# Optimization experiments

Hardware: AMD Instinct MI355X
Metric: run time of the kernel (lower is better)

The kernel has to match this reference:

```python
import jax, jax.numpy as jnp
from jax import lax
import numpy as np

L = 21                      # total_labels (incl. background class 0)
VARIANCES = (0.1, 0.1, 0.2, 0.2)
NMS_THRESHOLD = 0.5
MAX_TOTAL_SIZE = 200        # also max_output_size_per_class
SCORE_THRESHOLD = 0.5


def setup_inputs() -> dict:
    key = jax.random.key(0)
    k1, k2, k3, k4 = jax.random.split(key, 4)
    B, N = 1, 2048
    # valid normalized rois: y1<y2, x1<x2, inside [0,1]
    yx = jax.random.uniform(k1, (B, N, 2)) * 0.8
    hw = jax.random.uniform(k2, (B, N, 2)) * 0.19 + 0.01
    roi_bboxes = jnp.concatenate([yx, yx + hw], axis=-1)
    pred_deltas = jax.random.normal(k3, (B, N, L * 4)) * 0.2
    pred_label_probs = jax.random.uniform(k4, (B, N, L))
    return {"roi_bboxes": roi_bboxes, "pred_deltas": pred_deltas,
            "pred_label_probs": pred_label_probs}


def _decode(rois, deltas):
    # rois/deltas: (..., 4), boxes [y1,x1,y2,x2], deltas [dy,dx,dh,dw]
    h = rois[..., 2] - rois[..., 0]
    w = rois[..., 3] - rois[..., 1]
    cy = rois[..., 0] + 0.5 * h
    cx = rois[..., 1] + 0.5 * w
    nh = jnp.exp(deltas[..., 2]) * h
    nw = jnp.exp(deltas[..., 3]) * w
    ncy = deltas[..., 0] * h + cy
    ncx = deltas[..., 1] * w + cx
    return jnp.stack([ncy - 0.5 * nh, ncx - 0.5 * nw,
                      ncy + 0.5 * nh, ncx + 0.5 * nw], axis=-1)


def _iou_matrix(b):  # b: (N,4) -> (N,N)
    y1, x1, y2, x2 = b[:, 0], b[:, 1], b[:, 2], b[:, 3]
    area = (y2 - y1) * (x2 - x1)
    ih = jnp.clip(jnp.minimum(y2[:, None], y2[None, :]) - jnp.maximum(y1[:, None], y1[None, :]), 0.0)
    iw = jnp.clip(jnp.minimum(x2[:, None], x2[None, :]) - jnp.maximum(x1[:, None], x1[None, :]), 0.0)
    inter = ih * iw
    return inter / (area[:, None] + area[None, :] - inter + 1e-9)


def _nms_sorted(boxes, scores):
    # greedy per-class NMS; returns boxes/scores sorted by score desc + keep mask
    order = jnp.argsort(-scores)
    b = boxes[order]
    s = scores[order]
    iou = _iou_matrix(lax.stop_gradient(b))  # NMS decisions are non-differentiable
    n = b.shape[0]
    idx = jnp.arange(n)

    def body(i, keep):
        sup = keep[i] & (iou[i] > NMS_THRESHOLD) & (idx > i)
        return keep & jnp.logical_not(sup)

    keep = lax.fori_loop(0, n, body, jnp.ones((n,), bool))
    keep = keep & (jnp.cumsum(keep) <= MAX_TOTAL_SIZE)  # max_output_size_per_class
    return b, s, keep


def reference(roi_bboxes, pred_deltas, pred_label_probs):
    B, N, _ = roi_bboxes.shape  # B == 1 (module's slicing logic assumes it)
    deltas = pred_deltas.reshape(B, N, L, 4) * jnp.asarray(VARIANCES, pred_deltas.dtype)
    rois = jnp.broadcast_to(roi_bboxes[:, :, None, :], (B, N, L, 4))
    boxes = _decode(rois, deltas)  # (B,N,L,4)

    # zero out all class scores for rois whose argmax is background (class 0)
    am = jnp.argmax(pred_label_probs, axis=-1)
    scores = jnp.where((am != 0)[..., None], pred_label_probs, 0.0)

    boxes_c = jnp.transpose(boxes[0], (1, 0, 2))  # (L,N,4)
    scores_c = scores[0].T                         # (L,N)
    b_s, s_s, keep = jax.vmap(_nms_sorted)(boxes_c, scores_c)

    cls = jnp.broadcast_to(jnp.arange(L, dtype=s_s.dtype)[:, None], (L, N))
    flat_b = b_s.reshape(-1, 4)
    flat_s = s_s.reshape(-1)
    flat_c = cls.reshape(-1)

    def select(kmask):
        sc = jnp.where(kmask.reshape(-1), flat_s, -1.0)
        top_sc, top_idx = lax.top_k(sc, MAX_TOTAL_SIZE)
        return top_sc, jnp.clip(flat_b[top_idx], 0.0, 1.0), flat_c[top_idx]

    # thresholded combined NMS result (padded with zeros, like TF CNMS)
    sc_t, b_t, l_t = select(keep & (s_s > SCORE_THRESHOLD))
    valid_t = sc_t > SCORE_THRESHOLD
    out_b = jnp.where(valid_t[:, None], b_t, 0.0)
    out_s = jnp.where(valid_t, sc_t, 0.0)
    out_l = jnp.where(valid_t, l_t, 0.0)

    # fallback: no detections above threshold -> best unthresholded detection
    sc_u, b_u, l_u = select(keep)
    best = sc_u[0]
    have = best >= 0.001
    slot0 = jnp.arange(MAX_TOTAL_SIZE) == 0
    fb_b = jnp.where((slot0 & have)[:, None], b_u[0], 0.0)
    fb_s = jnp.where(slot0 & have, best, 0.0)
    fb_l = jnp.where(slot0 & have, l_u[0], 0.0)

    use_fb = jnp.sum(valid_t) == 0
    fin_b = jnp.where(use_fb, fb_b, out_b)[None]  # (1, MAX_TOTAL_SIZE, 4)
    fin_s = jnp.where(use_fb, fb_s, out_s)[None]  # (1, MAX_TOTAL_SIZE)
    fin_l = jnp.where(use_fb, fb_l, out_l)[None]  # (1, MAX_TOTAL_SIZE)
    return fin_b, fin_l, fin_s
```

## Files before the change

### kernel.cpp

```cpp
#include <hip/hip_runtime.h>
#include <stdint.h>

#define NN 2048
#define LL 21
#define CAP 200
#define TOT (LL * CAP)
#define TMAX 320
#define NCH (TMAX / 64)
#define NBK 1024
#define ARRCAP 1200

typedef unsigned long long u64;
typedef unsigned int u32;

__device__ __forceinline__ u64 shfl_u64(u64 v, int lane) {
    int lo = (int)(u32)(v & 0xFFFFFFFFull);
    int hi = (int)(u32)(v >> 32);
    lo = __shfl(lo, lane);
    hi = __shfl(hi, lane);
    return ((u64)(u32)hi << 32) | (u32)lo;
}

__device__ __forceinline__ u64 shfl_xor_u64(u64 v, int mask) {
    int lo = (int)(u32)(v & 0xFFFFFFFFull);
    int hi = (int)(u32)(v >> 32);
    lo = __shfl_xor(lo, mask);
    hi = __shfl_xor(hi, mask);
    return ((u64)(u32)hi << 32) | (u32)lo;
}

__device__ __forceinline__ float4 clip01(float4 b) {
    b.x = fminf(fmaxf(b.x, 0.0f), 1.0f);
    b.y = fminf(fmaxf(b.y, 0.0f), 1.0f);
    b.z = fminf(fmaxf(b.z, 0.0f), 1.0f);
    b.w = fminf(fmaxf(b.w, 0.0f), 1.0f);
    return b;
}

__device__ __forceinline__ float4 decode_box(const float4 roi, const float4 dd) {
#pragma clang fp contract(off)
    float h  = roi.z - roi.x;
    float w  = roi.w - roi.y;
    float cy = roi.x + 0.5f * h;
    float cx = roi.y + 0.5f * w;
    float d0 = dd.x * 0.1f;
    float d1 = dd.y * 0.1f;
    float d2 = dd.z * 0.2f;
    float d3 = dd.w * 0.2f;
    float nh = (float)exp((double)d2) * h;
    float nw = (float)exp((double)d3) * w;
    float ncy = d0 * h + cy;
    float ncx = d1 * w + cx;
    return make_float4(ncy - 0.5f * nh, ncx - 0.5f * nw, ncy + 0.5f * nh, ncx + 0.5f * nw);
}

__device__ __forceinline__ float area_of(const float4 b) {
#pragma clang fp contract(off)
    return (b.z - b.x) * (b.w - b.y);
}

__device__ __forceinline__ bool iou_gt(const float4 a, const float4 b) {
#pragma clang fp contract(off)
    float areaA = (a.z - a.x) * (a.w - a.y);
    float areaB = (b.z - b.x) * (b.w - b.y);
    float ih = fminf(a.z, b.z) - fmaxf(a.x, b.x);
    ih = fmaxf(ih, 0.0f);
    float iw = fminf(a.w, b.w) - fmaxf(a.y, b.y);
    iw = fmaxf(iw, 0.0f);
    float inter = ih * iw;
    float denom = ((areaA + areaB) - inter) + 1e-9f;
    return (inter / denom) > 0.5f;
}

__device__ __forceinline__ bool iou_gt_pre(const float4 a, const float4 b,
                                           float areaA, float areaB) {
#pragma clang fp contract(off)
    float ih = fminf(a.z, b.z) - fmaxf(a.x, b.x);
    ih = fmaxf(ih, 0.0f);
    float iw = fminf(a.w, b.w) - fmaxf(a.y, b.y);
    iw = fmaxf(iw, 0.0f);
    float inter = ih * iw;
    float denom = ((areaA + areaB) - inter) + 1e-9f;
    return (inter / denom) > 0.5f;
}

__device__ __forceinline__ int rb_of(u64 key) {
    u32 sb = (u32)(key >> 32);
    int rb = 1023 - (int)((sb - 0x3F000000u) >> 13);
    return min(max(rb, 0), 1023);
}

__device__ __forceinline__ u64 lowmask(int n) {
    return (n >= 64) ? ~0ull : ((1ull << n) - 1ull);
}

__device__ __forceinline__ void desc_scan(int* histR, int* dstart, int* cursor,
                                          int* wtot, int t, int nthr) {
    const int PB = NBK / nthr;
    const int lane = t & 63, w = t >> 6;
    int c[4], local = 0;
    for (int k = 0; k < PB; ++k) { c[k] = histR[PB * t + k]; local += c[k]; }
    int incl = local;
    for (int d = 1; d < 64; d <<= 1) {
        int v = __shfl_up(incl, d);
        if (lane >= d) incl += v;
    }
    if (lane == 63) wtot[w] = incl;
    __syncthreads();
    int woff = 0;
    for (int i = 0; i < w; ++i) woff += wtot[i];
    int run = woff + incl - local;
    for (int k = 0; k < PB; ++k) {
        dstart[PB * t + k] = run;
        cursor[PB * t + k] = run;
        run += c[k];
    }
    __syncthreads();
}

__global__ __launch_bounds__(256) void score_kernel(
    const float* __restrict__ probs,
    u32* __restrict__ scoreT)
{
    __shared__ float tile[256 * LL];
    const int a0 = blockIdx.x * 256;
    const int t = threadIdx.x;
    const float4* src = (const float4*)probs + blockIdx.x * 1344;
    float4* dst = (float4*)tile;
    for (int i = t; i < 1344; i += 256) dst[i] = src[i];
    __syncthreads();
    const float* row = tile + t * LL;
    float best = row[0];
    int bi = 0;
    for (int j = 1; j < LL; ++j) {
        float v = row[j];
        if (v > best) { best = v; bi = j; }
    }
    for (int c = 0; c < LL; ++c)
        scoreT[c * NN + a0 + t] = (bi != 0) ? __float_as_uint(row[c]) : 0u;
}

#define SMEM_B 64384
#define A1OFF 17408
#define A2OFF 34816
#define A3OFF 47104
#define A4OFF 63104

__global__ __launch_bounds__(512) void per_class_kernel(
    const u32* __restrict__ scoreT,
    const float* __restrict__ roi,
    const float* __restrict__ deltas,
    u64* __restrict__ cand_key,
    float4* __restrict__ cand_box,
    u64* __restrict__ fb_key,
    float4* __restrict__ fb_box,
    int* __restrict__ ctr,
    float* __restrict__ out)
{
    const int cls = blockIdx.x;
    const int t = threadIdx.x;
    const int lane = t & 63;

    __shared__ char sm[SMEM_B];
    __shared__ int sCnt, sK, sLast, sRbstar;
    __shared__ u64 sGmax;
    __shared__ u64 keepm[NCH];
    __shared__ int wtot[8];

    u64* skey  = (u64*)sm;
    u64* skey3 = (u64*)sm;
    u64* skey2 = (u64*)(sm + A1OFF);
    int* histR  = (int*)(sm + A2OFF);
    int* cursor = (int*)(sm + A2OFF + 4096);
    int* dstart = (int*)(sm + A2OFF + 8192);
    float4* cbox = (float4*)(sm + A3OFF);
    u64* R  = (u64*)(sm + A3OFF + 5120);
    u64* Tm = (u64*)(sm + A3OFF + 7680);
    float4* kept = (float4*)(sm + A3OFF + 12800);
    float* area = (float*)(sm + A4OFF);

    if (t == 0) { sCnt = 0; sK = 0; sGmax = 0ull; }
    for (int s = t; s < CAP; s += 512) cand_key[cls * CAP + s] = 0ull;
    for (int i = t; i < NBK; i += 512) histR[i] = 0;
    __syncthreads();

    uint4 s4 = ((const uint4*)(scoreT + cls * NN))[t];
    u32 sv[4] = { s4.x, s4.y, s4.z, s4.w };
    u64 lq[4];
    int ln = 0;
    u64 lmax = 0ull;
    for (int k = 0; k < 4; ++k) {
        u32 a = 4 * t + k;
        u64 key = ((u64)sv[k] << 32) | (u32)(~a);
        if (key > lmax) lmax = key;
        if (sv[k] > 0x3F000000u) lq[ln++] = key;
    }
    for (int d = 1; d < 64; d <<= 1) {
        u64 o = shfl_xor_u64(lmax, d);
        if (o > lmax) lmax = o;
    }
    if (lane == 0) atomicMax(&sGmax, lmax);
    int incl = ln;
    for (int d = 1; d < 64; d <<= 1) {
        int v = __shfl_up(incl, d);
        if (lane >= d) incl += v;
    }
    int wsum = __shfl(incl, 63);
    int wbase = 0;
    if (lane == 63) wbase = atomicAdd(&sCnt, wsum);
    wbase = __shfl(wbase, 63);
    int off = wbase + incl - ln;
    for (int j = 0; j < ln; ++j) {
        skey[off + j] = lq[j];
        atomicAdd(&histR[rb_of(lq[j])], 1);
    }
    __syncthreads();
    const int M = sCnt;
    const int TT = min(M, TMAX);

    if (t == 0) {
        u64 g = sGmax;
        u32 a0 = ~(u32)(g & 0xFFFFFFFFull);
        float4 rb = *(const float4*)(roi + a0 * 4);
        float4 dd = *(const float4*)(deltas + a0 * (LL * 4) + cls * 4);
        fb_box[cls] = decode_box(rb, dd);
        fb_key[cls] = (g & 0xFFFFFFFF00000000ull) | (u32)(~(u32)(cls * NN));
    }

    desc_scan(histR, dstart, cursor, wtot, t, 512);

    for (int i = t; i < M; i += 512) {
        u64 k = skey[i];
        int pos = atomicAdd(&cursor[rb_of(k)], 1);
        skey2[pos] = k;
    }
    __syncthreads();

    for (int p = t; p < M; p += 512) {
        u64 k = skey2[p];
        int rb = rb_of(k);
        int s = dstart[rb], e = s + histR[rb];
        int rnk = s;
        for (int q = s; q < e; ++q) rnk += (skey2[q] > k) ? 1 : 0;
        skey3[rnk] = k;
        if (rnk < TT) {
            u32 a = ~(u32)(k & 0xFFFFFFFFull);
            float4 rbx = *(const float4*)(roi + a * 4);
            float4 dd = *(const float4*)(deltas + a * (LL * 4) + cls * 4);
            float4 bx = decode_box(rbx, dd);
            cbox[rnk] = bx;
            area[rnk] = area_of(bx);
        }
    }
    __syncthreads();

    const int NCHe = (TT + 63) / 64;
    const int NJ = NCHe * (NCHe + 1) / 2;

    for (int task = t; task < NJ * 64; task += 512) {
        const int jobid = task >> 6, j = task & 63;
        int cj = 0, acc = 0;
        while (acc + cj + 1 <= jobid) { acc += cj + 1; ++cj; }
        const int ci = jobid - acc;
        const int gj = cj * 64 + j;
        const int nbj = min(64, TT - cj * 64);
        if (ci == cj) {
            u64 row = 0ull;
            if (j < nbj) {
                float4 bj = cbox[gj];
                float aj = area[gj];
                for (int r2 = j + 1; r2 < nbj; ++r2)
                    if (iou_gt_pre(bj, cbox[cj * 64 + r2], aj, area[cj * 64 + r2]))
                        row |= (1ull << r2);
            }
            R[cj * 64 + j] = row;
        } else {
            u64 wd = 0ull;
            if (j < nbj) {
                float4 bj = cbox[gj];
                float aj = area[gj];
                const float4* cb = cbox + ci * 64;
                const float* ca = area + ci * 64;
                for (int i = 0; i < 64; ++i)
                    if (iou_gt_pre(cb[i], bj, ca[i], aj)) wd |= (1ull << i);
            }
            Tm[(cj * (cj - 1) / 2 + ci) * 64 + j] = wd;
        }
    }
    __syncthreads();

    if (t < 64) {
        int K = 0;
        for (int cj = 0; cj < NCHe; ++cj) {
            if (K >= CAP) break;
            const int nb = min(64, TT - cj * 64);
            u64 row = R[cj * 64 + t];
            bool ext = (t >= nb);
            for (int ci = 0; ci < cj; ++ci)
                if (Tm[(cj * (cj - 1) / 2 + ci) * 64 + t] & keepm[ci]) ext = true;
            u64 rem = __ballot(ext);
            const u64 nz = __ballot(row != 0ull) & ~rem;
            u64 m = nz;
            while (m) {
                int i = __ffsll(m) - 1;
                u64 ri = shfl_u64(row, i);
                rem |= ri;
                u64 gt = (i == 63) ? 0ull : ~lowmask(i + 1);
                m = nz & ~rem & gt;
            }
            u64 keep = ~rem & lowmask(nb);
            if (t == 0) keepm[cj] = keep;
            if (t < nb && ((keep >> t) & 1ull)) {
                int krank = K + __popcll(keep & lowmask(t));
                if (krank < CAP) {
                    kept[krank] = cbox[cj * 64 + t];
                    int slot = cls * CAP + krank;
                    cand_key[slot] = (skey3[cj * 64 + t] & 0xFFFFFFFF00000000ull) |
                                     (u32)(~(u32)slot);
                    cand_box[slot] = cbox[cj * 64 + t];
                }
            }
            K += __popcll(keep);
        }
        if (t == 0) sK = K;
    }
    __syncthreads();

    int K = sK;
    if (K < CAP && M > TT) {
        u64* sup = (u64*)(sm + A3OFF + 5120);
        unsigned char* extq = (unsigned char*)(sm + A3OFF + 9216);
        const int g = t >> 6, r = t & 63;
        for (int base = TT; base < M; base += 64) {
            K = sK;
            if (K >= CAP) break;
            const int nb = min(64, M - base);
            if (t < nb) {
                u32 a = ~(u32)(skey3[base + t] & 0xFFFFFFFFull);
                float4 rbx = *(const float4*)(roi + a * 4);
                float4 dd = *(const float4*)(deltas + a * (LL * 4) + cls * 4);
                cbox[t] = decode_box(rbx, dd);
            }
            __syncthreads();
            u64 bits = 0ull;
            if (r < nb) {
                float4 br = cbox[r];
                int lo = max(r + 1, g * 8), hi = min(nb, (g + 1) * 8);
                for (int r2 = lo; r2 < hi; ++r2)
                    if (iou_gt(br, cbox[r2])) bits |= (1ull << r2);
            }
            sup[g * 64 + r] = bits;
            bool f = false;
            if (r < nb) {
                float4 bm = cbox[r];
                int per = (K + 7) >> 3;
                int e0 = g * per, e1 = min(K, e0 + per);
                for (int e = e0; e < e1; ++e)
                    if (iou_gt(kept[e], bm)) { f = true; break; }
            }
            extq[g * 64 + r] = f ? 1 : 0;
            __syncthreads();
            if (t < 64) {
                u64 row = 0ull;
                int extv = 0;
                for (int j = 0; j < 8; ++j) { row |= sup[j * 64 + t]; extv |= extq[j * 64 + t]; }
                bool ext = (t < nb) ? (extv != 0) : true;
                u64 rem = __ballot(ext);
                const u64 nz = __ballot(row != 0ull) & ~rem;
                u64 m = nz;
                while (m) {
                    int i = __ffsll(m) - 1;
                    u64 ri = shfl_u64(row, i);
                    rem |= ri;
                    u64 gt = (i == 63) ? 0ull : ~lowmask(i + 1);
                    m = nz & ~rem & gt;
                }
                u64 keep = ~rem & lowmask(nb);
                if (t < nb && ((keep >> t) & 1ull)) {
                    int krank = K + __popcll(keep & lowmask(t));
                    if (krank < CAP) {
                        kept[krank] = cbox[t];
                        int slot = cls * CAP + krank;
                        cand_key[slot] = (skey3[base + t] & 0xFFFFFFFF00000000ull) |
                                         (u32)(~(u32)slot);
                        cand_box[slot] = cbox[t];
                    }
                }
                if (t == 0) sK = K + __popcll(keep);
            }
            __syncthreads();
        }
    }

    __threadfence();
    if (t == 0) {
        int old = __hip_atomic_fetch_add(ctr, 1, __ATOMIC_ACQ_REL, __HIP_MEMORY_SCOPE_AGENT);
        sLast = (old == LL - 1) ? 1 : 0;
        sRbstar = NBK - 1;
    }
    __syncthreads();
    if (!sLast) return;

    {
        u64* keys = (u64*)sm;
        u64* arr  = (u64*)(sm + A3OFF);
        u64* outk = (u64*)(sm + A3OFF + 9600);

        for (int i = t; i < NBK; i += 512) histR[i] = 0;
        for (int i = t; i < CAP; i += 512) outk[i] = 0ull;
        __syncthreads();

        for (int i = t; i < TOT; i += 512) {
            u64 k = __hip_atomic_load(&cand_key[i], __ATOMIC_RELAXED,
                                      __HIP_MEMORY_SCOPE_AGENT);
            keys[i] = k;
            if (k != 0ull) atomicAdd(&histR[rb_of(k)], 1);
        }
        __syncthreads();
        desc_scan(histR, dstart, cursor, wtot, t, 512);
        for (int k = 0; k < 2; ++k) {
            int rb = 2 * t + k;
            if (dstart[rb] < CAP && dstart[rb] + histR[rb] >= CAP) sRbstar = rb;
        }
        __syncthreads();
        const int rbstar = sRbstar;

        for (int i = t; i < TOT; i += 512) {
            u64 k = keys[i];
            if (k != 0ull) {
                int rb = rb_of(k);
                if (rb <= rbstar) {
                    int pos = atomicAdd(&cursor[rb], 1);
                    if (pos < ARRCAP) arr[pos] = k;
                }
            }
        }
        __syncthreads();

        const int E = min(dstart[rbstar] + histR[rbstar], ARRCAP);
        for (int p = t; p < E; p += 512) {
            u64 k = arr[p];
            int rb = rb_of(k);
            int s = dstart[rb], e = min(s + histR[rb], ARRCAP);
            int rnk = s;
            for (int q = s; q < e; ++q) rnk += (arr[q] > k) ? 1 : 0;
            if (rnk < CAP) outk[rnk] = k;
        }
        __syncthreads();

        for (int o = t; o < CAP; o += 512) {
            u64 key = outk[o];
            float4 b = make_float4(0.0f, 0.0f, 0.0f, 0.0f);
            float lab = 0.0f, sc = 0.0f;
            if (key != 0ull) {
                u32 slot = ~(u32)(key & 0xFFFFFFFFull);
                sc = __uint_as_float((u32)(key >> 32));
                lab = (float)(slot / CAP);
                const u64* bp = (const u64*)&cand_box[slot];
                u64 w0 = __hip_atomic_load(bp,     __ATOMIC_RELAXED, __HIP_MEMORY_SCOPE_AGENT);
                u64 w1 = __hip_atomic_load(bp + 1, __ATOMIC_RELAXED, __HIP_MEMORY_SCOPE_AGENT);
                float4 bb;
                ((u64*)&bb)[0] = w0;
                ((u64*)&bb)[1] = w1;
                b = clip01(bb);
            }
            out[o * 4 + 0] = b.x;
            out[o * 4 + 1] = b.y;
            out[o * 4 + 2] = b.z;
            out[o * 4 + 3] = b.w;
            out[4 * CAP + o] = lab;
            out[5 * CAP + o] = sc;
        }
        __syncthreads();

        if (t == 0 && outk[0] == 0ull) {
            u64 best = 0ull;
            int bc = 0;
            for (int c = 0; c < LL; ++c) {
                u64 k = __hip_atomic_load(&fb_key[c], __ATOMIC_RELAXED,
                                          __HIP_MEMORY_SCOPE_AGENT);
                if (k > best) { best = k; bc = c; }
            }
            float bs = __uint_as_float((u32)(best >> 32));
            if (bs >= 0.001f) {
                const u64* bp = (const u64*)&fb_box[bc];
                u64 w0 = __hip_atomic_load(bp,     __ATOMIC_RELAXED, __HIP_MEMORY_SCOPE_AGENT);
                u64 w1 = __hip_atomic_load(bp + 1, __ATOMIC_RELAXED, __HIP_MEMORY_SCOPE_AGENT);
                float4 bb;
                ((u64*)&bb)[0] = w0;
                ((u64*)&bb)[1] = w1;
                bb = clip01(bb);
                out[0] = bb.x; out[1] = bb.y; out[2] = bb.z; out[3] = bb.w;
                out[4 * CAP] = (float)bc;
                out[5 * CAP] = bs;
            }
        }
    }
}

extern "C" void kernel_launch(void* const* d_in, const int* in_sizes, int n_in,
                              void* d_out, int out_size, void* d_ws, size_t ws_size,
                              hipStream_t stream) {
    const float* roi    = (const float*)d_in[0];
    const float* deltas = (const float*)d_in[1];
    const float* probs  = (const float*)d_in[2];
    float* out = (float*)d_out;

    char* ws = (char*)d_ws;
    u32*    scoreT   = (u32*)ws;
    u64*    cand_key = (u64*)(ws + 172032);
    float4* cand_box = (float4*)(ws + 205632);
    u64*    fb_key   = (u64*)(ws + 272832);
    float4* fb_box   = (float4*)(ws + 273008);
    int*    ctr      = (int*)(ws + 273344);

    (void)hipMemsetAsync(ctr, 0, 4, stream);
    score_kernel<<<NN / 256, 256, 0, stream>>>(probs, scoreT);
    per_class_kernel<<<LL, 512, 0, stream>>>(scoreT, roi, deltas,
                                             cand_key, cand_box, fb_key, fb_box,
                                             ctr, out);
}
```

Before: 94.93 us.

## Fuse score kernel into per-class kernel with grid-wide barrier on foreground mask

Removes the separate score/transpose kernel. Each of the 21 blocks computes the argmax-foreground bits for a slice of anchors and publishes them as a ballot bitmask. All blocks then spin on a global counter until every block has finished. Each block afterwards reads its class column of probabilities directly with strided loads, gated by the shared mask. This drops one kernel launch and the transposed score buffer, at the cost of a spin barrier that needs all 21 blocks to be co-resident and of uncoalesced strided reads of probs.

```diff
diff --git a/kernel.cpp b/kernel.cpp
--- a/kernel.cpp
+++ b/kernel.cpp
@@ -95,11 +95,10 @@
 }
 
 __device__ __forceinline__ void desc_scan(int* histR, int* dstart, int* cursor,
-                                          int* wtot, int t, int nthr) {
-    const int PB = NBK / nthr;
+                                          int* wtot, int t) {
     const int lane = t & 63, w = t >> 6;
-    int c[4], local = 0;
-    for (int k = 0; k < PB; ++k) { c[k] = histR[PB * t + k]; local += c[k]; }
+    int c[2], local = 0;
+    for (int k = 0; k < 2; ++k) { c[k] = histR[2 * t + k]; local += c[k]; }
     int incl = local;
     for (int d = 1; d < 64; d <<= 1) {
         int v = __shfl_up(incl, d);
@@ -110,34 +109,12 @@
     int woff = 0;
     for (int i = 0; i < w; ++i) woff += wtot[i];
     int run = woff + incl - local;
-    for (int k = 0; k < PB; ++k) {
-        dstart[PB * t + k] = run;
-        cursor[PB * t + k] = run;
+    for (int k = 0; k < 2; ++k) {
+        dstart[2 * t + k] = run;
+        cursor[2 * t + k] = run;
         run += c[k];
     }
     __syncthreads();
-}
-
-__global__ __launch_bounds__(256) void score_kernel(
-    const float* __restrict__ probs,
-    u32* __restrict__ scoreT)
-{
-    __shared__ float tile[256 * LL];
-    const int a0 = blockIdx.x * 256;
-    const int t = threadIdx.x;
-    const float4* src = (const float4*)probs + blockIdx.x * 1344;
-    float4* dst = (float4*)tile;
-    for (int i = t; i < 1344; i += 256) dst[i] = src[i];
-    __syncthreads();
-    const float* row = tile + t * LL;
-    float best = row[0];
-    int bi = 0;
-    for (int j = 1; j < LL; ++j) {
-        float v = row[j];
-        if (v > best) { best = v; bi = j; }
-    }
-    for (int c = 0; c < LL; ++c)
-        scoreT[c * NN + a0 + t] = (bi != 0) ? __float_as_uint(row[c]) : 0u;
 }
 
 #define SMEM_B 64384
@@ -146,15 +123,16 @@
 #define A3OFF 47104
 #define A4OFF 63104
 
-__global__ __launch_bounds__(512) void per_class_kernel(
-    const u32* __restrict__ scoreT,
+__global__ __launch_bounds__(512) void fused_kernel(
+    const float* __restrict__ probs,
     const float* __restrict__ roi,
     const float* __restrict__ deltas,
     u64* __restrict__ cand_key,
     float4* __restrict__ cand_box,
     u64* __restrict__ fb_key,
     float4* __restrict__ fb_box,
-    int* __restrict__ ctr,
+    u32* __restrict__ ctr,
+    u64* __restrict__ fgmask,
     float* __restrict__ out)
 {
     const int cls = blockIdx.x;
@@ -166,6 +144,7 @@
     __shared__ u64 sGmax;
     __shared__ u64 keepm[NCH];
     __shared__ int wtot[8];
+    __shared__ u64 sFg[NN / 64];
 
     u64* skey  = (u64*)sm;
     u64* skey3 = (u64*)sm;
@@ -182,18 +161,56 @@
     if (t == 0) { sCnt = 0; sK = 0; sGmax = 0ull; }
     for (int s = t; s < CAP; s += 512) cand_key[cls * CAP + s] = 0ull;
     for (int i = t; i < NBK; i += 512) histR[i] = 0;
-    __syncthreads();
-
-    uint4 s4 = ((const uint4*)(scoreT + cls * NN))[t];
-    u32 sv[4] = { s4.x, s4.y, s4.z, s4.w };
+
+    {
+        const int w0 = (cls < 11) ? 2 * cls : cls + 11;
+        const int nw = (cls < 11) ? 2 : 1;
+        const int a0 = w0 * 64;
+        const int cnt = nw * 64 * LL;
+        float* tile = (float*)sm;
+        for (int i = t; i < cnt; i += 512) tile[i] = probs[a0 * LL + i];
+        __syncthreads();
+        bool fg = false;
+        if (t < nw * 64) {
+            const float* row = tile + t * LL;
+            float best = row[0];
+            int bi = 0;
+            for (int j = 1; j < LL; ++j) {
+                float v = row[j];
+                if (v > best) { best = v; bi = j; }
+            }
+            fg = (bi != 0);
+        }
+        u64 word = __ballot(fg);
+        const int wv = t >> 6;
+        if (lane == 0 && wv < nw) fgmask[w0 + wv] = word;
+        __syncthreads();
+    }
+
+    __threadfence();
+    if (t == 0) {
+        __hip_atomic_fetch_add(&ctr[0], 1u, __ATOMIC_ACQ_REL, __HIP_MEMORY_SCOPE_AGENT);
+        while (__hip_atomic_load(&ctr[0], __ATOMIC_ACQUIRE, __HIP_MEMORY_SCOPE_AGENT) < (u32)LL) {}
+    }
+    __syncthreads();
+    if (t < NN / 64)
+        sFg[t] = __hip_atomic_load(&fgmask[t], __ATOMIC_RELAXED, __HIP_MEMORY_SCOPE_AGENT);
+    __syncthreads();
+
     u64 lq[4];
     int ln = 0;
     u64 lmax = 0ull;
-    for (int k = 0; k < 4; ++k) {
-        u32 a = 4 * t + k;
-        u64 key = ((u64)sv[k] << 32) | (u32)(~a);
-        if (key > lmax) lmax = key;
-        if (sv[k] > 0x3F000000u) lq[ln++] = key;
+    {
+        float v[4];
+        for (int k = 0; k < 4; ++k) v[k] = probs[(4 * t + k) * LL + cls];
+        for (int k = 0; k < 4; ++k) {
+            u32 a = 4 * t + k;
+            bool fg = (sFg[a >> 6] >> (a & 63)) & 1ull;
+            u32 sb = fg ? __float_as_uint(v[k]) : 0u;
+            u64 key = ((u64)sb << 32) | (u32)(~a);
+            if (key > lmax) lmax = key;
+            if (sb > 0x3F000000u) lq[ln++] = key;
+        }
     }
     for (int d = 1; d < 64; d <<= 1) {
         u64 o = shfl_xor_u64(lmax, d);
@@ -202,8 +219,8 @@
     if (lane == 0) atomicMax(&sGmax, lmax);
     int incl = ln;
     for (int d = 1; d < 64; d <<= 1) {
-        int v = __shfl_up(incl, d);
-        if (lane >= d) incl += v;
+        int v2 = __shfl_up(incl, d);
+        if (lane >= d) incl += v2;
     }
     int wsum = __shfl(incl, 63);
     int wbase = 0;
@@ -227,7 +244,7 @@
         fb_key[cls] = (g & 0xFFFFFFFF00000000ull) | (u32)(~(u32)(cls * NN));
     }
 
-    desc_scan(histR, dstart, cursor, wtot, t, 512);
+    desc_scan(histR, dstart, cursor, wtot, t);
 
     for (int i = t; i < M; i += 512) {
         u64 k = skey[i];
@@ -394,8 +411,9 @@
 
     __threadfence();
     if (t == 0) {
-        int old = __hip_atomic_fetch_add(ctr, 1, __ATOMIC_ACQ_REL, __HIP_MEMORY_SCOPE_AGENT);
-        sLast = (old == LL - 1) ? 1 : 0;
+        u32 old = __hip_atomic_fetch_add(&ctr[1], 1u, __ATOMIC_ACQ_REL,
+                                         __HIP_MEMORY_SCOPE_AGENT);
+        sLast = (old == (u32)(LL - 1)) ? 1 : 0;
         sRbstar = NBK - 1;
     }
     __syncthreads();
@@ -417,7 +435,7 @@
             if (k != 0ull) atomicAdd(&histR[rb_of(k)], 1);
         }
         __syncthreads();
-        desc_scan(histR, dstart, cursor, wtot, t, 512);
+        desc_scan(histR, dstart, cursor, wtot, t);
         for (int k = 0; k < 2; ++k) {
             int rb = 2 * t + k;
             if (dstart[rb] < CAP && dstart[rb] + histR[rb] >= CAP) sRbstar = rb;
@@ -507,16 +525,15 @@
     float* out = (float*)d_out;
 
     char* ws = (char*)d_ws;
-    u32*    scoreT   = (u32*)ws;
-    u64*    cand_key = (u64*)(ws + 172032);
-    float4* cand_box = (float4*)(ws + 205632);
-    u64*    fb_key   = (u64*)(ws + 272832);
-    float4* fb_box   = (float4*)(ws + 273008);
-    int*    ctr      = (int*)(ws + 273344);
-
-    (void)hipMemsetAsync(ctr, 0, 4, stream);
-    score_kernel<<<NN / 256, 256, 0, stream>>>(probs, scoreT);
-    per_class_kernel<<<LL, 512, 0, stream>>>(scoreT, roi, deltas,
-                                             cand_key, cand_box, fb_key, fb_box,
-                                             ctr, out);
-}
+    u64*    cand_key = (u64*)ws;
+    float4* cand_box = (float4*)(ws + 33600);
+    u64*    fb_key   = (u64*)(ws + 100800);
+    float4* fb_box   = (float4*)(ws + 100976);
+    u32*    ctr      = (u32*)(ws + 101312);
+    u64*    fgmask   = (u64*)(ws + 101320);
+
+    (void)hipMemsetAsync(ctr, 0, 8, stream);
+    fused_kernel<<<LL, 512, 0, stream>>>(probs, roi, deltas,
+                                         cand_key, cand_box, fb_key, fb_box,
+                                         ctr, fgmask, out);
+}
```

Result: slower. 98.96 us (+4.2%).

## Split final top-k into separate kernel and double per-class block threads

Applied to the files above, without the earlier changes.

The per-class NMS kernel now runs 1024 threads per block instead of 512, so each thread handles two scores and the extension-phase work is split across 16 waves. The last-block-done atomic counter handshake and its memset are removed, and the final cross-class top-k and output writing move into a new single-block kernel launched afterwards. This drops the global fence and atomic traffic, but adds one kernel launch and puts scratch arrays at new shared-memory offsets.

```diff
diff --git a/kernel.cpp b/kernel.cpp
--- a/kernel.cpp
+++ b/kernel.cpp
@@ -94,11 +94,13 @@
     return (n >= 64) ? ~0ull : ((1ull << n) - 1ull);
 }
 
+template <int NTHR>
 __device__ __forceinline__ void desc_scan(int* histR, int* dstart, int* cursor,
-                                          int* wtot, int t, int nthr) {
-    const int PB = NBK / nthr;
+                                          int* wtot, int t) {
+    const int PB = NBK / NTHR;
+    const int NW = NTHR / 64;
     const int lane = t & 63, w = t >> 6;
-    int c[4], local = 0;
+    int c[PB], local = 0;
     for (int k = 0; k < PB; ++k) { c[k] = histR[PB * t + k]; local += c[k]; }
     int incl = local;
     for (int d = 1; d < 64; d <<= 1) {
@@ -108,7 +110,7 @@
     if (lane == 63) wtot[w] = incl;
     __syncthreads();
     int woff = 0;
-    for (int i = 0; i < w; ++i) woff += wtot[i];
+    for (int i = 0; i < w && i < NW; ++i) woff += wtot[i];
     int run = woff + incl - local;
     for (int k = 0; k < PB; ++k) {
         dstart[PB * t + k] = run;
@@ -146,26 +148,24 @@
 #define A3OFF 47104
 #define A4OFF 63104
 
-__global__ __launch_bounds__(512) void per_class_kernel(
+__global__ __launch_bounds__(1024, 1) void per_class_kernel(
     const u32* __restrict__ scoreT,
     const float* __restrict__ roi,
     const float* __restrict__ deltas,
     u64* __restrict__ cand_key,
     float4* __restrict__ cand_box,
     u64* __restrict__ fb_key,
-    float4* __restrict__ fb_box,
-    int* __restrict__ ctr,
-    float* __restrict__ out)
+    float4* __restrict__ fb_box)
 {
     const int cls = blockIdx.x;
     const int t = threadIdx.x;
     const int lane = t & 63;
 
     __shared__ char sm[SMEM_B];
-    __shared__ int sCnt, sK, sLast, sRbstar;
+    __shared__ int sCnt, sK;
     __shared__ u64 sGmax;
     __shared__ u64 keepm[NCH];
-    __shared__ int wtot[8];
+    __shared__ int wtot[16];
 
     u64* skey  = (u64*)sm;
     u64* skey3 = (u64*)sm;
@@ -180,17 +180,17 @@
     float* area = (float*)(sm + A4OFF);
 
     if (t == 0) { sCnt = 0; sK = 0; sGmax = 0ull; }
-    for (int s = t; s < CAP; s += 512) cand_key[cls * CAP + s] = 0ull;
-    for (int i = t; i < NBK; i += 512) histR[i] = 0;
-    __syncthreads();
-
-    uint4 s4 = ((const uint4*)(scoreT + cls * NN))[t];
-    u32 sv[4] = { s4.x, s4.y, s4.z, s4.w };
-    u64 lq[4];
+    if (t < CAP) cand_key[cls * CAP + t] = 0ull;
+    histR[t] = 0;
+    __syncthreads();
+
+    uint2 s2 = ((const uint2*)(scoreT + cls * NN))[t];
+    u32 sv[2] = { s2.x, s2.y };
+    u64 lq[2];
     int ln = 0;
     u64 lmax = 0ull;
-    for (int k = 0; k < 4; ++k) {
-        u32 a = 4 * t + k;
+    for (int k = 0; k < 2; ++k) {
+        u32 a = 2 * t + k;
         u64 key = ((u64)sv[k] << 32) | (u32)(~a);
         if (key > lmax) lmax = key;
         if (sv[k] > 0x3F000000u) lq[ln++] = key;
@@ -227,16 +227,16 @@
         fb_key[cls] = (g & 0xFFFFFFFF00000000ull) | (u32)(~(u32)(cls * NN));
     }
 
-    desc_scan(histR, dstart, cursor, wtot, t, 512);
-
-    for (int i = t; i < M; i += 512) {
+    desc_scan<1024>(histR, dstart, cursor, wtot, t);
+
+    for (int i = t; i < M; i += 1024) {
         u64 k = skey[i];
         int pos = atomicAdd(&cursor[rb_of(k)], 1);
         skey2[pos] = k;
     }
     __syncthreads();
 
-    for (int p = t; p < M; p += 512) {
+    for (int p = t; p < M; p += 1024) {
         u64 k = skey2[p];
         int rb = rb_of(k);
         int s = dstart[rb], e = s + histR[rb];
@@ -257,7 +257,7 @@
     const int NCHe = (TT + 63) / 64;
     const int NJ = NCHe * (NCHe + 1) / 2;
 
-    for (int task = t; task < NJ * 64; task += 512) {
+    for (int task = t; task < NJ * 64; task += 1024) {
         const int jobid = task >> 6, j = task & 63;
         int cj = 0, acc = 0;
         while (acc + cj + 1 <= jobid) { acc += cj + 1; ++cj; }
@@ -328,8 +328,8 @@
 
     int K = sK;
     if (K < CAP && M > TT) {
-        u64* sup = (u64*)(sm + A3OFF + 5120);
-        unsigned char* extq = (unsigned char*)(sm + A3OFF + 9216);
+        u64* sup = (u64*)(sm + A1OFF);
+        unsigned char* extq = (unsigned char*)(sm + A1OFF + 8192);
         const int g = t >> 6, r = t & 63;
         for (int base = TT; base < M; base += 64) {
             K = sK;
@@ -345,7 +345,7 @@
             u64 bits = 0ull;
             if (r < nb) {
                 float4 br = cbox[r];
-                int lo = max(r + 1, g * 8), hi = min(nb, (g + 1) * 8);
+                int lo = max(r + 1, g * 4), hi = min(nb, (g + 1) * 4);
                 for (int r2 = lo; r2 < hi; ++r2)
                     if (iou_gt(br, cbox[r2])) bits |= (1ull << r2);
             }
@@ -353,7 +353,7 @@
             bool f = false;
             if (r < nb) {
                 float4 bm = cbox[r];
-                int per = (K + 7) >> 3;
+                int per = (K + 15) >> 4;
                 int e0 = g * per, e1 = min(K, e0 + per);
                 for (int e = e0; e < e1; ++e)
                     if (iou_gt(kept[e], bm)) { f = true; break; }
@@ -363,7 +363,7 @@
             if (t < 64) {
                 u64 row = 0ull;
                 int extv = 0;
-                for (int j = 0; j < 8; ++j) { row |= sup[j * 64 + t]; extv |= extq[j * 64 + t]; }
+                for (int j = 0; j < 16; ++j) { row |= sup[j * 64 + t]; extv |= extq[j * 64 + t]; }
                 bool ext = (t < nb) ? (extv != 0) : true;
                 u64 rem = __ballot(ext);
                 const u64 nz = __ballot(row != 0ull) & ~rem;
@@ -391,109 +391,100 @@
             __syncthreads();
         }
     }
-
-    __threadfence();
-    if (t == 0) {
-        int old = __hip_atomic_fetch_add(ctr, 1, __ATOMIC_ACQ_REL, __HIP_MEMORY_SCOPE_AGENT);
-        sLast = (old == LL - 1) ? 1 : 0;
-        sRbstar = NBK - 1;
-    }
-    __syncthreads();
-    if (!sLast) return;
-
-    {
-        u64* keys = (u64*)sm;
-        u64* arr  = (u64*)(sm + A3OFF);
-        u64* outk = (u64*)(sm + A3OFF + 9600);
-
-        for (int i = t; i < NBK; i += 512) histR[i] = 0;
-        for (int i = t; i < CAP; i += 512) outk[i] = 0ull;
-        __syncthreads();
-
-        for (int i = t; i < TOT; i += 512) {
-            u64 k = __hip_atomic_load(&cand_key[i], __ATOMIC_RELAXED,
-                                      __HIP_MEMORY_SCOPE_AGENT);
-            keys[i] = k;
-            if (k != 0ull) atomicAdd(&histR[rb_of(k)], 1);
-        }
-        __syncthreads();
-        desc_scan(histR, dstart, cursor, wtot, t, 512);
-        for (int k = 0; k < 2; ++k) {
-            int rb = 2 * t + k;
-            if (dstart[rb] < CAP && dstart[rb] + histR[rb] >= CAP) sRbstar = rb;
-        }
-        __syncthreads();
-        const int rbstar = sRbstar;
-
-        for (int i = t; i < TOT; i += 512) {
-            u64 k = keys[i];
-            if (k != 0ull) {
-                int rb = rb_of(k);
-                if (rb <= rbstar) {
-                    int pos = atomicAdd(&cursor[rb], 1);
-                    if (pos < ARRCAP) arr[pos] = k;
-                }
-            }
-        }
-        __syncthreads();
-
-        const int E = min(dstart[rbstar] + histR[rbstar], ARRCAP);
-        for (int p = t; p < E; p += 512) {
-            u64 k = arr[p];
+}
+
+__global__ __launch_bounds__(512) void topk_kernel(
+    const u64* __restrict__ cand_key,
+    const float4* __restrict__ cand_box,
+    const u64* __restrict__ fb_key,
+    const float4* __restrict__ fb_box,
+    float* __restrict__ out)
+{
+    const int t = threadIdx.x;
+    __shared__ u64 keys[TOT];
+    __shared__ int histR[NBK], cursor[NBK], dstart[NBK];
+    __shared__ u64 arr[ARRCAP];
+    __shared__ u64 outk[CAP];
+    __shared__ int wtot[8];
+    __shared__ int sRbstar;
+
+    for (int i = t; i < NBK; i += 512) histR[i] = 0;
+    if (t < CAP) outk[t] = 0ull;
+    if (t == 0) sRbstar = NBK - 1;
+    __syncthreads();
+
+    const ulong2* ck2 = (const ulong2*)cand_key;
+    for (int i = t; i < TOT / 2; i += 512) {
+        ulong2 k2 = ck2[i];
+        keys[2 * i]     = k2.x;
+        keys[2 * i + 1] = k2.y;
+        if (k2.x != 0ull) atomicAdd(&histR[rb_of(k2.x)], 1);
+        if (k2.y != 0ull) atomicAdd(&histR[rb_of(k2.y)], 1);
+    }
+    __syncthreads();
+    desc_scan<512>(histR, dstart, cursor, wtot, t);
+    for (int k = 0; k < 2; ++k) {
+        int rb = 2 * t + k;
+        if (dstart[rb] < CAP && dstart[rb] + histR[rb] >= CAP) sRbstar = rb;
+    }
+    __syncthreads();
+    const int rbstar = sRbstar;
+
+    for (int i = t; i < TOT; i += 512) {
+        u64 k = keys[i];
+        if (k != 0ull) {
             int rb = rb_of(k);
-            int s = dstart[rb], e = min(s + histR[rb], ARRCAP);
-            int rnk = s;
-            for (int q = s; q < e; ++q) rnk += (arr[q] > k) ? 1 : 0;
-            if (rnk < CAP) outk[rnk] = k;
-        }
-        __syncthreads();
-
-        for (int o = t; o < CAP; o += 512) {
-            u64 key = outk[o];
-            float4 b = make_float4(0.0f, 0.0f, 0.0f, 0.0f);
-            float lab = 0.0f, sc = 0.0f;
-            if (key != 0ull) {
-                u32 slot = ~(u32)(key & 0xFFFFFFFFull);
-                sc = __uint_as_float((u32)(key >> 32));
-                lab = (float)(slot / CAP);
-                const u64* bp = (const u64*)&cand_box[slot];
-                u64 w0 = __hip_atomic_load(bp,     __ATOMIC_RELAXED, __HIP_MEMORY_SCOPE_AGENT);
-                u64 w1 = __hip_atomic_load(bp + 1, __ATOMIC_RELAXED, __HIP_MEMORY_SCOPE_AGENT);
-                float4 bb;
-                ((u64*)&bb)[0] = w0;
-                ((u64*)&bb)[1] = w1;
-                b = clip01(bb);
-            }
-            out[o * 4 + 0] = b.x;
-            out[o * 4 + 1] = b.y;
-            out[o * 4 + 2] = b.z;
-            out[o * 4 + 3] = b.w;
-            out[4 * CAP + o] = lab;
-            out[5 * CAP + o] = sc;
-        }
-        __syncthreads();
-
-        if (t == 0 && outk[0] == 0ull) {
-            u64 best = 0ull;
-            int bc = 0;
-            for (int c = 0; c < LL; ++c) {
-                u64 k = __hip_atomic_load(&fb_key[c], __ATOMIC_RELAXED,
-                                          __HIP_MEMORY_SCOPE_AGENT);
-                if (k > best) { best = k; bc = c; }
-            }
-            float bs = __uint_as_float((u32)(best >> 32));
-            if (bs >= 0.001f) {
-                const u64* bp = (const u64*)&fb_box[bc];
-                u64 w0 = __hip_atomic_load(bp,     __ATOMIC_RELAXED, __HIP_MEMORY_SCOPE_AGENT);
-                u64 w1 = __hip_atomic_load(bp + 1, __ATOMIC_RELAXED, __HIP_MEMORY_SCOPE_AGENT);
-                float4 bb;
-                ((u64*)&bb)[0] = w0;
-                ((u64*)&bb)[1] = w1;
-                bb = clip01(bb);
-                out[0] = bb.x; out[1] = bb.y; out[2] = bb.z; out[3] = bb.w;
-                out[4 * CAP] = (float)bc;
-                out[5 * CAP] = bs;
-            }
+            if (rb <= rbstar) {
+                int pos = atomicAdd(&cursor[rb], 1);
+                if (pos < ARRCAP) arr[pos] = k;
+            }
+        }
+    }
+    __syncthreads();
+
+    const int E = min(dstart[rbstar] + histR[rbstar], ARRCAP);
+    for (int p = t; p < E; p += 512) {
+        u64 k = arr[p];
+        int rb = rb_of(k);
+        int s = dstart[rb], e = min(s + histR[rb], ARRCAP);
+        int rnk = s;
+        for (int q = s; q < e; ++q) rnk += (arr[q] > k) ? 1 : 0;
+        if (rnk < CAP) outk[rnk] = k;
+    }
+    __syncthreads();
+
+    for (int o = t; o < CAP; o += 512) {
+        u64 key = outk[o];
+        float4 b = make_float4(0.0f, 0.0f, 0.0f, 0.0f);
+        float lab = 0.0f, sc = 0.0f;
+        if (key != 0ull) {
+            u32 slot = ~(u32)(key & 0xFFFFFFFFull);
+            sc = __uint_as_float((u32)(key >> 32));
+            lab = (float)(slot / CAP);
+            b = clip01(cand_box[slot]);
+        }
+        out[o * 4 + 0] = b.x;
+        out[o * 4 + 1] = b.y;
+        out[o * 4 + 2] = b.z;
+        out[o * 4 + 3] = b.w;
+        out[4 * CAP + o] = lab;
+        out[5 * CAP + o] = sc;
+    }
+    __syncthreads();
+
+    if (t == 0 && outk[0] == 0ull) {
+        u64 best = 0ull;
+        int bc = 0;
+        for (int c = 0; c < LL; ++c) {
+            u64 k = fb_key[c];
+            if (k > best) { best = k; bc = c; }
+        }
+        float bs = __uint_as_float((u32)(best >> 32));
+        if (bs >= 0.001f) {
+            float4 bb = clip01(fb_box[bc]);
+            out[0] = bb.x; out[1] = bb.y; out[2] = bb.z; out[3] = bb.w;
+            out[4 * CAP] = (float)bc;
+            out[5 * CAP] = bs;
         }
     }
 }
@@ -512,11 +503,9 @@
     float4* cand_box = (float4*)(ws + 205632);
     u64*    fb_key   = (u64*)(ws + 272832);
     float4* fb_box   = (float4*)(ws + 273008);
-    int*    ctr      = (int*)(ws + 273344);
-
-    (void)hipMemsetAsync(ctr, 0, 4, stream);
+
     score_kernel<<<NN / 256, 256, 0, stream>>>(probs, scoreT);
-    per_class_kernel<<<LL, 512, 0, stream>>>(scoreT, roi, deltas,
-                                             cand_key, cand_box, fb_key, fb_box,
-                                             ctr, out);
-}
+    per_class_kernel<<<LL, 1024, 0, stream>>>(scoreT, roi, deltas,
+                                              cand_key, cand_box, fb_key, fb_box);
+    topk_kernel<<<1, 512, 0, stream>>>(cand_key, cand_box, fb_key, fb_box, out);
+}
```

Result: faster. 87.63 us, median of 2 (-7.7%).
